# Performance work log

Hardware: AMD Instinct MI355X
Metric: run time of the kernel (lower is better)

## Reference

```python
import jax, jax.numpy as jnp
import numpy as np

EPS = 0.1   # module __init__ default eps
TAU = 1.0   # map_em default tau


def _mog_eval(pi, mu, Sigma, data):
    # pi: (B,p), mu/Sigma: (B,p,d), data: (B,N,d)
    d = data.shape[-1]
    inv_S = 1.0 / Sigma
    jll = -0.5 * (
        d * jnp.log(2.0 * jnp.pi)
        + jnp.log(Sigma).sum(-1)[:, None, :]                      # (B,1,p)
        + jnp.einsum('bnd,bpd->bnp', data * data, inv_S)          # Mahalanobis x^2 term
        + (mu * mu * inv_S).sum(-1)[:, None, :]                   # mu^2/Sigma term
        - 2.0 * jnp.einsum('bnd,bpd->bnp', data, mu * inv_S)      # cross term
    ) + jnp.log(pi)[:, None, :]
    mll = jax.nn.logsumexp(jll, axis=-1)          # (B,N)
    cll = jll - mll[..., None]                    # (B,N,p)
    return jll, cll, mll


def _map_m_step(data, weight, m, V, tau):
    # data: (B,N,d), weight: (B,N,p), m/V: (p,d)
    wsum = weight.sum(1)                                  # (B,p)
    wsum_reg = wsum + tau
    wxsum = jnp.einsum('bnp,bnd->bpd', weight, data)
    wxxsum = jnp.einsum('bnp,bnd->bpd', weight, data * data)
    pi = wsum_reg / wsum_reg.sum(1, keepdims=True)
    mu = (wxsum + m[None] * tau) / wsum_reg[..., None]
    Sigma = (wxxsum + (V + m * m)[None] * tau) / wsum_reg[..., None] - mu * mu
    return pi, mu, Sigma


def setup_inputs() -> dict:
    key = jax.random.key(0)
    k1, k2 = jax.random.split(key)
    B, N, d, p = 8, 4096, 1024, 16
    data = jax.random.normal(k1, (B, N, d), dtype=jnp.float32)
    mask = jnp.ones((B, N), dtype=jnp.float32)
    m = 0.1 * jax.random.normal(k2, (p, d), dtype=jnp.float32)
    V_ = jnp.full((p, d), np.log(np.e - 1.0), dtype=jnp.float32)
    return {"data": data, "mask": mask, "m": m, "V_": V_, "num_iters": 3}


def reference(data, mask, m, V_, num_iters):
    B, N, d = data.shape
    p = m.shape[0]
    # prior (DirNIWNet.forward + mode)
    V = EPS * jax.nn.softplus(V_)
    pi = jnp.full((B, p), 1.0 / p, dtype=data.dtype)
    mu = jnp.broadcast_to(m, (B, p, d)).astype(data.dtype)
    Sigma = jnp.broadcast_to(V, (B, p, d)).astype(data.dtype)
    qq = jnp.zeros((B, N, p), dtype=data.dtype)
    for _ in range(num_iters):  # small fixed iteration count (EM)
        _, cll, _ = _mog_eval(pi, mu, Sigma, data)
        qq = jnp.exp(cll) * mask[..., None]
        pi, mu, Sigma = _map_m_step(data, qq, m, V, TAU)
    return pi, mu, Sigma, qq
```

## Files before the change

kernel.cpp:

```cpp
#include <hip/hip_runtime.h>
#include <math.h>

#define BB 8
#define NN 4096
#define DD 1024
#define PP 16
#define KS 8
#define KC (DD / KS)

static constexpr float DLOG2PI = 1881.9861160031696f;
static constexpr float EPSC = 0.1f;


#define FELEM(v, c) ((c) == 0 ? (v).x : (c) == 1 ? (v).y : (c) == 2 ? (v).z : (v).w)

__global__ __launch_bounds__(256) void k_init(const float* __restrict__ m,
                                              const float* __restrict__ V_,
                                              float* __restrict__ Wmat,
                                              float* __restrict__ cns)
{
    int j = blockIdx.x, b = blockIdx.y;
    int tid = threadIdx.x;
    __shared__ float red[512];
    int d0 = tid * 4;
    float4 m4 = *(const float4*)(m + j * DD + d0);
    float4 v4 = *(const float4*)(V_ + j * DD + d0);
    float mv[4] = {m4.x, m4.y, m4.z, m4.w};
    float vv[4] = {v4.x, v4.y, v4.z, v4.w};
    float* Wb = Wmat + (size_t)b * (DD * 32);
    float llog = 0.f, lmq = 0.f;
#pragma unroll
    for (int c = 0; c < 4; c++) {
        float V = EPSC * log1pf(expf(vv[c]));
        float inv = 1.0f / V;
        int d = d0 + c;
        Wb[d * 32 + j * 2] = inv;
        Wb[d * 32 + j * 2 + 1] = mv[c] * inv;
        llog += logf(V);
        lmq += mv[c] * mv[c] * inv;
    }
    red[tid] = llog; red[256 + tid] = lmq;
    __syncthreads();
    for (int s = 128; s > 0; s >>= 1) {
        if (tid < s) { red[tid] += red[tid + s]; red[256 + tid] += red[256 + tid + s]; }
        __syncthreads();
    }
    if (tid == 0)
        cns[b * PP + j] = logf(1.0f / 16.0f) - 0.5f * (DLOG2PI + red[0] + red[256]);
}

__global__ __launch_bounds__(256) void k_estep(const float* __restrict__ X,
                                               const float* __restrict__ Wmat,
                                               float* __restrict__ epart)
{
    int rb = blockIdx.x, ks = blockIdx.y, b = blockIdx.z;
    int tid = threadIdx.x;
    int n0 = rb * 512 + tid * 2;
    const float* xp0 = X + ((size_t)b * NN + n0) * DD + ks * KC;
    const float* xp1 = xp0 + DD;
    const float* wp = Wmat + (size_t)b * (DD * 32) + (size_t)(ks * KC) * 32;
    float a1[2][16] = {};
    float a2[2][16] = {};
    float4 cur[8], nxt[8];

#define ESTEP_LOAD(BUF, T)                                                     \
    _Pragma("unroll")                                                          \
    for (int u = 0; u < 4; u++) {                                              \
        BUF[u]     = *(const float4*)(xp0 + (T) * 16 + u * 4);                 \
        BUF[4 + u] = *(const float4*)(xp1 + (T) * 16 + u * 4);                 \
    }

#define ESTEP_COMPUTE(BUF, T)                                                  \
    _Pragma("unroll")                                                          \
    for (int u = 0; u < 4; u++) {                                              \
        _Pragma("unroll")                                                      \
        for (int c = 0; c < 4; c++) {                                          \
            const float* wk = wp + ((T) * 16 + u * 4 + c) * 32;                \
            float xv0 = FELEM(BUF[u], c),     xq0 = xv0 * xv0;                 \
            float xv1 = FELEM(BUF[4 + u], c), xq1 = xv1 * xv1;                 \
            _Pragma("unroll")                                                  \
            for (int j = 0; j < 16; j++) {                                     \
                a1[0][j] = fmaf(xq0, wk[2 * j],     a1[0][j]);                 \
                a2[0][j] = fmaf(xv0, wk[2 * j + 1], a2[0][j]);                 \
                a1[1][j] = fmaf(xq1, wk[2 * j],     a1[1][j]);                 \
                a2[1][j] = fmaf(xv1, wk[2 * j + 1], a2[1][j]);                 \
            }                                                                  \
        }                                                                      \
    }

    ESTEP_LOAD(cur, 0)
#pragma unroll 1
    for (int t = 0; t < 8; t += 2) {
        ESTEP_LOAD(nxt, t + 1)
        ESTEP_COMPUTE(cur, t)
        int t2 = (t + 2 < 8) ? t + 2 : 0;
        ESTEP_LOAD(cur, t2)
        ESTEP_COMPUTE(nxt, t + 1)
    }
#undef ESTEP_LOAD
#undef ESTEP_COMPUTE

    float* ep = epart + (((size_t)ks * BB + b) * NN + n0) * PP;
#pragma unroll
    for (int r = 0; r < 2; r++) {
#pragma unroll
        for (int q = 0; q < 4; q++) {
            float4 v = make_float4(-0.5f * a1[r][q * 4 + 0] + a2[r][q * 4 + 0],
                                   -0.5f * a1[r][q * 4 + 1] + a2[r][q * 4 + 1],
                                   -0.5f * a1[r][q * 4 + 2] + a2[r][q * 4 + 2],
                                   -0.5f * a1[r][q * 4 + 3] + a2[r][q * 4 + 3]);
            *(float4*)(ep + r * PP + q * 4) = v;
        }
    }
}

__global__ __launch_bounds__(128) void k_ereduce(const float* __restrict__ epart,
                                                 const float* __restrict__ mask,
                                                 const float* __restrict__ cns,
                                                 float* __restrict__ qq,
                                                 float* __restrict__ wsum_p)
{
    int chunk = blockIdx.x, b = blockIdx.y;
    int tid = threadIdx.x;
    int n = chunk * 128 + tid;
    __shared__ float cs[16];
    __shared__ float red[128 * 17];
    if (tid < 16) cs[tid] = cns[b * PP + tid];
    __syncthreads();
    float jl[16];
#pragma unroll
    for (int q = 0; q < 4; q++) {
        float4 v = *(const float4*)(epart + ((size_t)b * NN + n) * PP + q * 4);
        jl[q * 4 + 0] = v.x; jl[q * 4 + 1] = v.y; jl[q * 4 + 2] = v.z; jl[q * 4 + 3] = v.w;
    }
#pragma unroll
    for (int ks = 1; ks < KS; ks++) {
#pragma unroll
        for (int q = 0; q < 4; q++) {
            float4 v = *(const float4*)(epart + (((size_t)ks * BB + b) * NN + n) * PP + q * 4);
            jl[q * 4 + 0] += v.x; jl[q * 4 + 1] += v.y; jl[q * 4 + 2] += v.z; jl[q * 4 + 3] += v.w;
        }
    }
    float mx = -3.4e38f;
#pragma unroll
    for (int j = 0; j < 16; j++) { jl[j] += cs[j]; mx = fmaxf(mx, jl[j]); }
    float sum = 0.f;
#pragma unroll
    for (int j = 0; j < 16; j++) { jl[j] = expf(jl[j] - mx); sum += jl[j]; }
    float r = mask[(size_t)b * NN + n] / sum;
    float* qo = qq + ((size_t)b * NN + n) * PP;
#pragma unroll
    for (int q = 0; q < 4; q++) {
        float4 v = make_float4(jl[q * 4 + 0] * r, jl[q * 4 + 1] * r,
                               jl[q * 4 + 2] * r, jl[q * 4 + 3] * r);
        *(float4*)(qo + q * 4) = v;
        red[tid * 17 + q * 4 + 0] = v.x;
        red[tid * 17 + q * 4 + 1] = v.y;
        red[tid * 17 + q * 4 + 2] = v.z;
        red[tid * 17 + q * 4 + 3] = v.w;
    }
    __syncthreads();
    if (tid < 16) {
        float s = 0.f;
#pragma unroll 8
        for (int t = 0; t < 128; t++) s += red[t * 17 + tid];
        wsum_p[((size_t)b * 32 + chunk) * 16 + tid] = s;
    }
}

__global__ __launch_bounds__(512) void k_mstep(const float* __restrict__ X,
                                               const float* __restrict__ qq,
                                               float* __restrict__ wxp,
                                               float* __restrict__ wxxp)
{
    int nq = blockIdx.x, b = blockIdx.y;
    int tid = threadIdx.x;
    int cg = tid & 255;
    int ph = tid >> 8;
    int col0 = cg * 4;
    const float* Xb = X + (size_t)b * NN * DD;
    const float* qb = qq + (size_t)b * NN * PP;
    int nbase = nq * 128 + ph;
    float aw[16][4] = {};
    float ax[16][4] = {};

#define MSTEP_FMA(XV, QP)                                                      \
    {                                                                          \
        float x2x = (XV).x * (XV).x, x2y = (XV).y * (XV).y;                    \
        float x2z = (XV).z * (XV).z, x2w = (XV).w * (XV).w;                    \
        _Pragma("unroll")                                                      \
        for (int j = 0; j < 16; j++) {                                         \
            float qj = (QP)[j];                                                \
            aw[j][0] = fmaf(qj, (XV).x, aw[j][0]);                             \
            aw[j][1] = fmaf(qj, (XV).y, aw[j][1]);                             \
            aw[j][2] = fmaf(qj, (XV).z, aw[j][2]);                             \
            aw[j][3] = fmaf(qj, (XV).w, aw[j][3]);                             \
            ax[j][0] = fmaf(qj, x2x, ax[j][0]);                                \
            ax[j][1] = fmaf(qj, x2y, ax[j][1]);                                \
            ax[j][2] = fmaf(qj, x2z, ax[j][2]);                                \
            ax[j][3] = fmaf(qj, x2w, ax[j][3]);                                \
        }                                                                      \
    }

    float4 xc = *(const float4*)(Xb + (size_t)nbase * DD + col0);
#pragma unroll 1
    for (int i = 0; i < 64; i += 2) {
        int na = nbase + i * 2;
        int nb_ = nbase + (i + 1) * 2;
        float4 xn = *(const float4*)(Xb + (size_t)nb_ * DD + col0);
        const float* q0 = qb + (size_t)na * PP;
        MSTEP_FMA(xc, q0)
        int i2 = (i + 2 < 64) ? i + 2 : 0;
        xc = *(const float4*)(Xb + (size_t)(nbase + i2 * 2) * DD + col0);
        const float* q1 = qb + (size_t)nb_ * PP;
        MSTEP_FMA(xn, q1)
    }
#undef MSTEP_FMA

    __shared__ float red[256 * 33];
#define MSTEP_PASS(SRC, JB, DST)                                               \
    __syncthreads();                                                           \
    if (ph == 1) {                                                             \
        _Pragma("unroll")                                                      \
        for (int jj = 0; jj < 8; jj++)                                         \
            *(float4*)(&red[cg * 33 + jj * 4]) =                               \
                make_float4(SRC[(JB) + jj][0], SRC[(JB) + jj][1],              \
                            SRC[(JB) + jj][2], SRC[(JB) + jj][3]);             \
    }                                                                          \
    __syncthreads();                                                           \
    if (ph == 0) {                                                             \
        _Pragma("unroll")                                                      \
        for (int jj = 0; jj < 8; jj++) {                                       \
            float4 o = *(float4*)(&red[cg * 33 + jj * 4]);                     \
            o.x += SRC[(JB) + jj][0];                                          \
            o.y += SRC[(JB) + jj][1];                                          \
            o.z += SRC[(JB) + jj][2];                                          \
            o.w += SRC[(JB) + jj][3];                                          \
            *(float4*)(DST + (((size_t)b * 32 + nq) * PP + (JB) + jj) * DD +   \
                       col0) = o;                                              \
        }                                                                      \
    }
    MSTEP_PASS(aw, 0, wxp)
    MSTEP_PASS(aw, 8, wxp)
    MSTEP_PASS(ax, 0, wxxp)
    MSTEP_PASS(ax, 8, wxxp)
#undef MSTEP_PASS
}

__global__ __launch_bounds__(256) void k_finalize(const float* __restrict__ wsum_p,
                                                  const float* __restrict__ wxp,
                                                  const float* __restrict__ wxxp,
                                                  const float* __restrict__ m,
                                                  const float* __restrict__ V_,
                                                  float* __restrict__ pi,
                                                  float* __restrict__ mu,
                                                  float* __restrict__ Sigma,
                                                  float* __restrict__ Wmat,
                                                  float* __restrict__ cns)
{
    int j = blockIdx.x, b = blockIdx.y;
    int tid = threadIdx.x;
    __shared__ float red[512];
    __shared__ float redw[16 * 17];
    __shared__ float wsr[16];
    __shared__ float sden;
    {
        int j2 = tid & 15, c2 = tid >> 4;
        float s = wsum_p[((size_t)b * 32 + 2 * c2) * 16 + j2]
                + wsum_p[((size_t)b * 32 + 2 * c2 + 1) * 16 + j2];
        redw[c2 * 17 + j2] = s;
    }
    __syncthreads();
    if (tid < 16) {
        float s = 0.f;
#pragma unroll
        for (int c2 = 0; c2 < 16; c2++) s += redw[c2 * 17 + tid];
        wsr[tid] = s + 1.0f;
    }
    __syncthreads();
    if (tid == 0) {
        float dd = 0.f;
#pragma unroll
        for (int jj = 0; jj < 16; jj++) dd += wsr[jj];
        sden = dd;
    }
    __syncthreads();
    float rws = 1.0f / wsr[j];
    float pij = wsr[j] / sden;
    int d0 = tid * 4;
    float wxa[4] = {0, 0, 0, 0}, wxxa[4] = {0, 0, 0, 0};
#pragma unroll
    for (int g = 0; g < 32; g++) {
        const float4 a = *(const float4*)(wxp + (((size_t)b * 32 + g) * PP + j) * DD + d0);
        wxa[0] += a.x; wxa[1] += a.y; wxa[2] += a.z; wxa[3] += a.w;
        const float4 c2 = *(const float4*)(wxxp + (((size_t)b * 32 + g) * PP + j) * DD + d0);
        wxxa[0] += c2.x; wxxa[1] += c2.y; wxxa[2] += c2.z; wxxa[3] += c2.w;
    }
    float4 m4 = *(const float4*)(m + j * DD + d0);
    float4 v4 = *(const float4*)(V_ + j * DD + d0);
    float mvv[4] = {m4.x, m4.y, m4.z, m4.w};
    float vvv[4] = {v4.x, v4.y, v4.z, v4.w};
    float muo[4], sgo[4];
    float llog = 0.f, lmq = 0.f;
    float* Wb = Wmat + (size_t)b * (DD * 32);
#pragma unroll
    for (int c = 0; c < 4; c++) {
        float V = EPSC * log1pf(expf(vvv[c]));
        float muv = (wxa[c] + mvv[c]) * rws;
        float Sg = (wxxa[c] + V + mvv[c] * mvv[c]) * rws - muv * muv;
        float inv = 1.0f / Sg;
        muo[c] = muv; sgo[c] = Sg;
        int d = d0 + c;
        Wb[d * 32 + j * 2] = inv;
        Wb[d * 32 + j * 2 + 1] = muv * inv;
        llog += logf(Sg);
        lmq += muv * muv * inv;
    }
    *(float4*)(mu + ((size_t)b * PP + j) * DD + d0) = make_float4(muo[0], muo[1], muo[2], muo[3]);
    *(float4*)(Sigma + ((size_t)b * PP + j) * DD + d0) = make_float4(sgo[0], sgo[1], sgo[2], sgo[3]);
    red[tid] = llog; red[256 + tid] = lmq;
    __syncthreads();
    for (int s = 128; s > 0; s >>= 1) {
        if (tid < s) { red[tid] += red[tid + s]; red[256 + tid] += red[256 + tid + s]; }
        __syncthreads();
    }
    if (tid == 0) {
        pi[b * PP + j] = pij;
        cns[b * PP + j] = logf(pij) - 0.5f * (DLOG2PI + red[0] + red[256]);
    }
}

extern "C" void kernel_launch(void* const* d_in, const int* in_sizes, int n_in,
                              void* d_out, int out_size, void* d_ws, size_t ws_size,
                              hipStream_t stream)
{
    (void)in_sizes; (void)n_in; (void)out_size; (void)ws_size;
    const float* data = (const float*)d_in[0];
    const float* mask = (const float*)d_in[1];
    const float* m    = (const float*)d_in[2];
    const float* V_   = (const float*)d_in[3];

    float* out = (float*)d_out;
    float* pi  = out;
    float* mu  = out + 128;
    float* Sg  = out + 128 + 131072;
    float* qq  = out + 128 + 2 * 131072;

    float* ws     = (float*)d_ws;
    float* Wmat   = ws;
    float* cns    = ws + 262144;
    float* epart  = ws + 262272;
    float* wxp    = ws + 262272 + 4194304;
    float* wxxp   = ws + 262272 + 2 * 4194304;
    float* wsum_p = ws + 262272 + 3 * 4194304;

    k_init<<<dim3(16, 8), 256, 0, stream>>>(m, V_, Wmat, cns);
    for (int it = 0; it < 3; it++) {
        k_estep<<<dim3(8, KS, 8), 256, 0, stream>>>(data, Wmat, epart);
        k_ereduce<<<dim3(32, 8), 128, 0, stream>>>(epart, mask, cns, qq, wsum_p);
        k_mstep<<<dim3(32, 8), 512, 0, stream>>>(data, qq, wxp, wxxp);
        k_finalize<<<dim3(16, 8), 256, 0, stream>>>(wsum_p, wxp, wxxp, m, V_, pi, mu, Sg, Wmat, cns);
    }
}
```

Baseline: 510.9 us.

## Stage data tiles through padded shared memory in E-step kernel

The E-step kernel now loads 256 rows by 32 columns of the data into a padded LDS tile with coalesced float4 loads, and each thread then computes one row from LDS. Before, each thread handled two rows and read its own strided float4 chunks straight from global memory with register double buffering. The grid doubles along the row axis so each block covers 256 rows instead of 512. The aim is better coalescing and more parallelism, at the cost of two barriers per tile, scalar LDS stores, and losing the two-row reuse of each weight load.

```diff
diff --git a/kernel.cpp b/kernel.cpp
--- a/kernel.cpp
+++ b/kernel.cpp
@@ -7,6 +7,7 @@
 #define PP 16
 #define KS 8
 #define KC (DD / KS)
+#define KT 32
 
 static constexpr float DLOG2PI = 1881.9861160031696f;
 static constexpr float EPSC = 0.1f;
@@ -55,62 +56,48 @@
 {
     int rb = blockIdx.x, ks = blockIdx.y, b = blockIdx.z;
     int tid = threadIdx.x;
-    int n0 = rb * 512 + tid * 2;
-    const float* xp0 = X + ((size_t)b * NN + n0) * DD + ks * KC;
-    const float* xp1 = xp0 + DD;
+    int n0 = rb * 256;
+    const float* Xb = X + ((size_t)b * NN + n0) * DD + ks * KC;
     const float* wp = Wmat + (size_t)b * (DD * 32) + (size_t)(ks * KC) * 32;
-    float a1[2][16] = {};
-    float a2[2][16] = {};
-    float4 cur[8], nxt[8];
-
-#define ESTEP_LOAD(BUF, T)                                                     \
-    _Pragma("unroll")                                                          \
-    for (int u = 0; u < 4; u++) {                                              \
-        BUF[u]     = *(const float4*)(xp0 + (T) * 16 + u * 4);                 \
-        BUF[4 + u] = *(const float4*)(xp1 + (T) * 16 + u * 4);                 \
-    }
-
-#define ESTEP_COMPUTE(BUF, T)                                                  \
-    _Pragma("unroll")                                                          \
-    for (int u = 0; u < 4; u++) {                                              \
-        _Pragma("unroll")                                                      \
-        for (int c = 0; c < 4; c++) {                                          \
-            const float* wk = wp + ((T) * 16 + u * 4 + c) * 32;                \
-            float xv0 = FELEM(BUF[u], c),     xq0 = xv0 * xv0;                 \
-            float xv1 = FELEM(BUF[4 + u], c), xq1 = xv1 * xv1;                 \
-            _Pragma("unroll")                                                  \
-            for (int j = 0; j < 16; j++) {                                     \
-                a1[0][j] = fmaf(xq0, wk[2 * j],     a1[0][j]);                 \
-                a2[0][j] = fmaf(xv0, wk[2 * j + 1], a2[0][j]);                 \
-                a1[1][j] = fmaf(xq1, wk[2 * j],     a1[1][j]);                 \
-                a2[1][j] = fmaf(xv1, wk[2 * j + 1], a2[1][j]);                 \
-            }                                                                  \
-        }                                                                      \
-    }
-
-    ESTEP_LOAD(cur, 0)
+    __shared__ float xs[256 * 33];
+    int srow = tid >> 3;
+    int sch = tid & 7;
+    float acc1[16] = {0,0,0,0,0,0,0,0,0,0,0,0,0,0,0,0};
+    float acc2[16] = {0,0,0,0,0,0,0,0,0,0,0,0,0,0,0,0};
 #pragma unroll 1
-    for (int t = 0; t < 8; t += 2) {
-        ESTEP_LOAD(nxt, t + 1)
-        ESTEP_COMPUTE(cur, t)
-        int t2 = (t + 2 < 8) ? t + 2 : 0;
-        ESTEP_LOAD(cur, t2)
-        ESTEP_COMPUTE(nxt, t + 1)
-    }
-#undef ESTEP_LOAD
-#undef ESTEP_COMPUTE
-
-    float* ep = epart + (((size_t)ks * BB + b) * NN + n0) * PP;
-#pragma unroll
-    for (int r = 0; r < 2; r++) {
-#pragma unroll
-        for (int q = 0; q < 4; q++) {
-            float4 v = make_float4(-0.5f * a1[r][q * 4 + 0] + a2[r][q * 4 + 0],
-                                   -0.5f * a1[r][q * 4 + 1] + a2[r][q * 4 + 1],
-                                   -0.5f * a1[r][q * 4 + 2] + a2[r][q * 4 + 2],
-                                   -0.5f * a1[r][q * 4 + 3] + a2[r][q * 4 + 3]);
-            *(float4*)(ep + r * PP + q * 4) = v;
+    for (int t = 0; t < KC / KT; t++) {
+        __syncthreads();
+#pragma unroll
+        for (int i = 0; i < 8; i++) {
+            int row = srow + i * 32;
+            float4 v = *(const float4*)(Xb + (size_t)row * DD + t * KT + sch * 4);
+            xs[row * 33 + sch * 4 + 0] = v.x;
+            xs[row * 33 + sch * 4 + 1] = v.y;
+            xs[row * 33 + sch * 4 + 2] = v.z;
+            xs[row * 33 + sch * 4 + 3] = v.w;
         }
+        __syncthreads();
+        const float* wt = wp + (size_t)(t * KT) * 32;
+#pragma unroll 8
+        for (int k = 0; k < KT; k++) {
+            float x = xs[tid * 33 + k];
+            float xq = x * x;
+            const float* wk = wt + k * 32;
+#pragma unroll
+            for (int j = 0; j < 16; j++) {
+                acc1[j] = fmaf(xq, wk[2 * j],     acc1[j]);
+                acc2[j] = fmaf(x,  wk[2 * j + 1], acc2[j]);
+            }
+        }
+    }
+    float* ep = epart + (((size_t)ks * BB + b) * NN + n0 + tid) * PP;
+#pragma unroll
+    for (int q = 0; q < 4; q++) {
+        float4 v = make_float4(-0.5f * acc1[q * 4 + 0] + acc2[q * 4 + 0],
+                               -0.5f * acc1[q * 4 + 1] + acc2[q * 4 + 1],
+                               -0.5f * acc1[q * 4 + 2] + acc2[q * 4 + 2],
+                               -0.5f * acc1[q * 4 + 3] + acc2[q * 4 + 3]);
+        *(float4*)(ep + q * 4) = v;
     }
 }
 
@@ -356,7 +343,7 @@
 
     k_init<<<dim3(16, 8), 256, 0, stream>>>(m, V_, Wmat, cns);
     for (int it = 0; it < 3; it++) {
-        k_estep<<<dim3(8, KS, 8), 256, 0, stream>>>(data, Wmat, epart);
+        k_estep<<<dim3(16, KS, 8), 256, 0, stream>>>(data, Wmat, epart);
         k_ereduce<<<dim3(32, 8), 128, 0, stream>>>(epart, mask, cns, qq, wsum_p);
         k_mstep<<<dim3(32, 8), 512, 0, stream>>>(data, qq, wxp, wxxp);
         k_finalize<<<dim3(16, 8), 256, 0, stream>>>(wsum_p, wxp, wxxp, m, V_, pi, mu, Sg, Wmat, cns);
```

Result: faster. 484.7 us (-5.1%).
